# Performance work log

Hardware: AMD Instinct MI355X
Metric: run time of the kernel (lower is better)

The kernel has to match this reference:

```python
import jax, jax.numpy as jnp
import numpy as np

LOG2PI = float(np.log(2.0 * np.pi))
T, S, D, K = 1024, 512, 32, 64


def setup_inputs() -> dict:
    key = jax.random.key(0)
    k0, k1, k2, k3, k4 = jax.random.split(key, 5)
    data = jax.random.normal(k0, (T, S, D), dtype=jnp.float32)  # packed time-major
    ip = jax.random.uniform(k1, (K,), dtype=jnp.float32)
    initial_probs = ip / ip.sum()
    A = jax.random.uniform(k2, (K, K), dtype=jnp.float32)
    transition_probs = A / A.sum(-1, keepdims=True)  # row-stochastic
    means = jax.random.normal(k3, (K, D), dtype=jnp.float32)
    covars = jax.random.uniform(k4, (K, D), dtype=jnp.float32) * 0.5 + 0.5  # positive diag
    return {"data": data, "initial_probs": initial_probs,
            "transition_probs": transition_probs, "means": means, "covars": covars}


def _emission_probs(data, means, covars):
    # Gaussian diag-covariance densities, [T, S, K], without materializing [T,S,K,D].
    inv = 1.0 / covars  # [K, D]
    quad = (jnp.einsum('tsd,kd->tsk', data * data, inv)
            - 2.0 * jnp.einsum('tsd,kd->tsk', data, means * inv)
            + (means * means * inv).sum(-1))  # [T, S, K]
    logp = -0.5 * (quad + jnp.log(covars).sum(-1) + data.shape[-1] * LOG2PI)
    return jnp.exp(logp)


def reference(data, initial_probs, transition_probs, means, covars):
    probs = _emission_probs(data, means, covars)  # [T, S, K]
    # t = 0: alpha = normalize(initial * emission)
    a0 = initial_probs * probs[0]
    d0 = a0.sum(-1, keepdims=True)
    alpha0 = a0 / d0
    log_denom0 = jnp.log(d0)  # [S, 1]

    def step(carry, p_t):
        alpha, log_denom = carry
        a = p_t * (alpha @ transition_probs)  # [S, K]
        d = a.sum(-1, keepdims=True)
        return (a / d, log_denom + jnp.log(d)), None

    (alpha, log_denom), _ = jax.lax.scan(step, (alpha0, log_denom0), probs[1:])
    log_likeli = jax.nn.logsumexp(jnp.log(alpha) + log_denom, axis=-1).sum()
    return alpha, -log_likeli
```

## Files before the change

kernel.cpp:

```cpp
#include <hip/hip_runtime.h>
#include <hip/hip_fp16.h>
#include <math.h>

#define TT 1024
#define SS 512
#define DD 32
#define KK 64

#define LOG2PI_F 1.8378770664093453f

#define NSEG 4
#define SEGLEN (TT / NSEG)
#define BURN 64


typedef float v2f __attribute__((ext_vector_type(2)));

__device__ __forceinline__ v2f fma2(v2f a, v2f b, v2f c) {
#if __has_builtin(__builtin_elementwise_fma)
    return __builtin_elementwise_fma(a, b, c);
#else
    v2f r; r.x = fmaf(a.x, b.x, c.x); r.y = fmaf(a.y, b.y, c.y); return r;
#endif
}

__device__ __forceinline__ void pin2(v2f& v) { asm volatile("" : "+v"(v)); }

template <int CTRL, int RMASK>
__device__ __forceinline__ float dpp_add(float x) {
    int t = __builtin_amdgcn_update_dpp(0, __float_as_int(x), CTRL, RMASK, 0xf, true);
    return x + __int_as_float(t);
}
template <int CTRL, int RMASK>
__device__ __forceinline__ float dpp_max(float x) {
    int xi = __float_as_int(x);
    int t = __builtin_amdgcn_update_dpp(xi, xi, CTRL, RMASK, 0xf, false);
    return fmaxf(x, __int_as_float(t));
}
__device__ __forceinline__ float wave_reduce_sum(float x) {
    x = dpp_add<0x111, 0xf>(x);
    x = dpp_add<0x112, 0xf>(x);
    x = dpp_add<0x114, 0xf>(x);
    x = dpp_add<0x118, 0xf>(x);
    x = dpp_add<0x142, 0xa>(x);
    x = dpp_add<0x143, 0xc>(x);
    return __int_as_float(__builtin_amdgcn_readlane(__float_as_int(x), 63));
}
__device__ __forceinline__ float wave_reduce_max(float x) {
    x = dpp_max<0x111, 0xf>(x);
    x = dpp_max<0x112, 0xf>(x);
    x = dpp_max<0x114, 0xf>(x);
    x = dpp_max<0x118, 0xf>(x);
    x = dpp_max<0x142, 0xa>(x);
    x = dpp_max<0x143, 0xc>(x);
    return __int_as_float(__builtin_amdgcn_readlane(__float_as_int(x), 63));
}

__global__ __launch_bounds__(64)
__attribute__((amdgpu_waves_per_eu(1, 2)))
void hmm_fused(
    const float* __restrict__ data,
    const float* __restrict__ initial,
    const float* __restrict__ trans,
    const float* __restrict__ means,
    const float* __restrict__ covars,
    float* __restrict__ out_alpha,
    float* __restrict__ seq_logd)
{
    const int s   = blockIdx.x;
    const int seg = blockIdx.y;
    const int k   = threadIdx.x;

    const int emit_from = seg * SEGLEN;
    const int t0        = seg ? (emit_from - BURN) : 0;
    const int nsteps    = seg ? (SEGLEN + BURN) : SEGLEN;

    v2f w2[DD / 2], m2[DD / 2];
    float c0 = DD * LOG2PI_F;
#pragma unroll
    for (int d = 0; d < DD; ++d) {
        float c = covars[k * DD + d];
        ((float*)w2)[d] = 1.0f / c;
        ((float*)m2)[d] = means[k * DD + d];
        c0 += __logf(c);
    }
#pragma unroll
    for (int j = 0; j < DD / 2; ++j) { pin2(w2[j]); pin2(m2[j]); }

    v2f acl[KK / 2];
#pragma unroll
    for (int j = 0; j < KK / 2; ++j) {
        acl[j].x = trans[(2 * j) * KK + k];
        acl[j].y = trans[(2 * j + 1) * KK + k];
    }
#pragma unroll
    for (int j = 0; j < KK / 2; ++j) pin2(acl[j]);

    __shared__ __align__(16) float alpha_sh[KK];

    float4 xA[DD / 4], xB[DD / 4];
    {
        const float4* xp = (const float4*)(data + ((size_t)t0 * SS + s) * DD);
#pragma unroll
        for (int j = 0; j < DD / 4; ++j) xA[j] = xp[j];
    }

    const float init_k = seg ? 1.0f : initial[k];
    float logd = 0.0f;
    float macc = 0.0f;
    float a = 0.0f;
    float scl = 1.0f;

#define FUSED_STEP(XCUR, XNXT, Ii)                                            \
    {                                                                         \
        const int t = t0 + 8 * mblk + (Ii);                                   \
        int tn = t + 1; if (tn >= TT) tn = TT - 1;         \
        const float4* xp =                                                    \
            (const float4*)(data + ((size_t)tn * SS + s) * DD);               \
        _Pragma("unroll")                                                     \
        for (int j = 0; j < DD / 4; ++j) XNXT[j] = xp[j];                     \
               \
        v2f q0 = {0.0f, 0.0f}, q1 = {0.0f, 0.0f};                             \
        _Pragma("unroll")                                                     \
        for (int d4 = 0; d4 < DD / 4; ++d4) {                                 \
            float4 x = XCUR[d4];                                              \
            v2f xa; xa.x = x.x; xa.y = x.y;                                   \
            v2f xb; xb.x = x.z; xb.y = x.w;                                   \
            v2f ta = xa - m2[2 * d4];                                         \
            v2f tb = xb - m2[2 * d4 + 1];                                     \
            q0 = fma2(w2[2 * d4] * ta, ta, q0);                               \
            q1 = fma2(w2[2 * d4 + 1] * tb, tb, q1);                           \
        }                                                                     \
        float qq = (q0.x + q0.y) + (q1.x + q1.y);                             \
        float logp = -0.5f * (qq + c0);                                       \
        float mx = wave_reduce_max(logp);              \
        float pc = __expf(logp - mx);                                         \
        if (((Ii) & 3) == 0) pc *= scl;            \
        if (t >= emit_from) macc += mx;                                       \
            \
        if ((Ii) == 0 && mblk == 0) {                                         \
            a = init_k * pc;                                                  \
        } else {                                                              \
            const float4* ash4 = (const float4*)alpha_sh;                     \
            v2f a0 = {0,0}, a1 = {0,0}, a2 = {0,0}, a3 = {0,0};               \
            _Pragma("unroll")                                                 \
            for (int j4 = 0; j4 < KK / 4; ++j4) {                             \
                float4 av = ash4[j4];                                         \
                v2f lo; lo.x = av.x; lo.y = av.y;                             \
                v2f hi; hi.x = av.z; hi.y = av.w;                             \
                if (j4 & 1) {                                                 \
                    a2 = fma2(lo, acl[2 * j4], a2);                           \
                    a3 = fma2(hi, acl[2 * j4 + 1], a3);                       \
                } else {                                                      \
                    a0 = fma2(lo, acl[2 * j4], a0);                           \
                    a1 = fma2(hi, acl[2 * j4 + 1], a1);                       \
                }                                                             \
            }                                                                 \
            v2f sv = (a0 + a1) + (a2 + a3);                                   \
            a = pc * (sv.x + sv.y);                                           \
        }                                                                     \
        alpha_sh[k] = a;                    \
        __builtin_amdgcn_wave_barrier();   \
        if (((Ii) & 3) == 3) {                \
            float den = wave_reduce_sum(a);                                   \
            logd += (t >= emit_from) ? __logf(den) : 0.0f;                    \
            scl = __builtin_amdgcn_rcpf(den);                                 \
        }                                                                     \
    }

    for (int mblk = 0; mblk < nsteps / 8; ++mblk) {
        FUSED_STEP(xA, xB, 0)
        FUSED_STEP(xB, xA, 1)
        FUSED_STEP(xA, xB, 2)
        FUSED_STEP(xB, xA, 3)
        FUSED_STEP(xA, xB, 4)
        FUSED_STEP(xB, xA, 5)
        FUSED_STEP(xA, xB, 6)
        FUSED_STEP(xB, xA, 7)
    }
#undef FUSED_STEP

    if (seg == NSEG - 1) out_alpha[(size_t)s * KK + k] = a * scl;
    if (k == 0) seq_logd[seg * SS + s] = logd + macc;
}

__global__ __launch_bounds__(256) void finalize(
    const float* __restrict__ seq_logd, float* __restrict__ out_nll)
{
    float v = 0.0f;
    for (int j = threadIdx.x; j < NSEG * SS; j += 256) v += seq_logd[j];
#pragma unroll
    for (int off = 32; off > 0; off >>= 1)
        v += __shfl_xor(v, off, 64);
    __shared__ float sh[4];
    if ((threadIdx.x & 63) == 0) sh[threadIdx.x >> 6] = v;
    __syncthreads();
    if (threadIdx.x == 0) {
        double total = ((double)sh[0] + sh[1]) + ((double)sh[2] + sh[3]);
        out_nll[0] = (float)(-total);
    }
}

extern "C" void kernel_launch(void* const* d_in, const int* in_sizes, int n_in,
                              void* d_out, int out_size, void* d_ws, size_t ws_size,
                              hipStream_t stream) {
    const float* data    = (const float*)d_in[0];
    const float* initial = (const float*)d_in[1];
    const float* trans   = (const float*)d_in[2];
    const float* means   = (const float*)d_in[3];
    const float* covars  = (const float*)d_in[4];

    float* out_alpha = (float*)d_out;
    float* out_nll   = (float*)d_out + (size_t)SS * KK;

    float* seq_logd = (float*)d_ws;

    hmm_fused<<<dim3(SS, NSEG), 64, 0, stream>>>(
        data, initial, trans, means, covars, out_alpha, seq_logd);
    finalize<<<1, 256, 0, stream>>>(seq_logd, out_nll);
}
```

Baseline: 301.3 us.

## Use readlane broadcast for alpha matvec and stage data through LDS double buffer

The alpha-times-transition matvec now broadcasts alpha with v_readlane from registers instead of writing it to shared memory and reading it back as float4. Each block of 8 timesteps of observation data is loaded cooperatively by the whole wave into a double-buffered LDS tile, replacing per-lane redundant float4 global loads. The segment count drops from 4 to 2 and the kernel is restricted to one wave per EU. This removes the LDS round trip and the redundant global traffic, but readlane produces scalar values, so the matvec may serialize through SGPRs. Fewer segments also means less parallelism and longer sequential chains per block.

Result: slower. 488.6 us (+62.2%).

```diff
diff --git a/kernel.cpp b/kernel.cpp
--- a/kernel.cpp
+++ b/kernel.cpp
@@ -1,5 +1,4 @@
 #include <hip/hip_runtime.h>
-#include <hip/hip_fp16.h>
 #include <math.h>
 
 #define TT 1024
@@ -9,7 +8,7 @@
 
 #define LOG2PI_F 1.8378770664093453f
 
-#define NSEG 4
+#define NSEG 2
 #define SEGLEN (TT / NSEG)
 #define BURN 64
 
@@ -25,6 +24,7 @@
 }
 
 __device__ __forceinline__ void pin2(v2f& v) { asm volatile("" : "+v"(v)); }
+__device__ __forceinline__ void pinf(float& v) { asm volatile("" : "+v"(v)); }
 
 template <int CTRL, int RMASK>
 __device__ __forceinline__ float dpp_add(float x) {
@@ -57,7 +57,7 @@
 }
 
 __global__ __launch_bounds__(64)
-__attribute__((amdgpu_waves_per_eu(1, 2)))
+__attribute__((amdgpu_waves_per_eu(1, 1)))
 void hmm_fused(
     const float* __restrict__ data,
     const float* __restrict__ initial,
@@ -87,43 +87,53 @@
 #pragma unroll
     for (int j = 0; j < DD / 2; ++j) { pin2(w2[j]); pin2(m2[j]); }
 
-    v2f acl[KK / 2];
-#pragma unroll
-    for (int j = 0; j < KK / 2; ++j) {
-        acl[j].x = trans[(2 * j) * KK + k];
-        acl[j].y = trans[(2 * j + 1) * KK + k];
-    }
-#pragma unroll
-    for (int j = 0; j < KK / 2; ++j) pin2(acl[j]);
-
-    __shared__ __align__(16) float alpha_sh[KK];
-
-    float4 xA[DD / 4], xB[DD / 4];
-    {
-        const float4* xp = (const float4*)(data + ((size_t)t0 * SS + s) * DD);
-#pragma unroll
-        for (int j = 0; j < DD / 4; ++j) xA[j] = xp[j];
-    }
+    float aclf[KK];
+#pragma unroll
+    for (int j = 0; j < KK; ++j) aclf[j] = trans[j * KK + k];
+#pragma unroll
+    for (int j = 0; j < KK; ++j) pinf(aclf[j]);
+
+    __shared__ __align__(16) float xlds[2][8 * DD];
+
+    const int half = k >> 5, d_lane = k & 31;
+    const float* xptr = data + (size_t)s * DD + (size_t)half * SS * DD + d_lane;
+
+    float xr0, xr1, xr2, xr3;
+#define XLOAD(TB)                                                             \
+    {                                                                         \
+        size_t bb = (size_t)(TB) * (SS * DD);                                 \
+        xr0 = xptr[bb];                                                       \
+        xr1 = xptr[bb + 2 * (SS * DD)];                                       \
+        xr2 = xptr[bb + 4 * (SS * DD)];                                       \
+        xr3 = xptr[bb + 6 * (SS * DD)];                                       \
+    }
+#define XWRITE(BUF)                                                           \
+    {                                                                         \
+        xlds[BUF][k]       = xr0;                                             \
+        xlds[BUF][64 + k]  = xr1;                                             \
+        xlds[BUF][128 + k] = xr2;                                             \
+        xlds[BUF][192 + k] = xr3;                                             \
+    }
+
+    XLOAD(t0);
+    XWRITE(0);
 
     const float init_k = seg ? 1.0f : initial[k];
     float logd = 0.0f;
     float macc = 0.0f;
     float a = 0.0f;
     float scl = 1.0f;
-
-#define FUSED_STEP(XCUR, XNXT, Ii)                                            \
+    int cur = 0;
+
+#define FUSED_STEP(Ii)                                                        \
     {                                                                         \
-        const int t = t0 + 8 * mblk + (Ii);                                   \
-        int tn = t + 1; if (tn >= TT) tn = TT - 1;         \
-        const float4* xp =                                                    \
-            (const float4*)(data + ((size_t)tn * SS + s) * DD);               \
-        _Pragma("unroll")                                                     \
-        for (int j = 0; j < DD / 4; ++j) XNXT[j] = xp[j];                     \
+        const int t = tbase + (Ii);                                           \
+        const float4* xq = (const float4*)(xcur + (Ii) * DD);                 \
                \
         v2f q0 = {0.0f, 0.0f}, q1 = {0.0f, 0.0f};                             \
         _Pragma("unroll")                                                     \
         for (int d4 = 0; d4 < DD / 4; ++d4) {                                 \
-            float4 x = XCUR[d4];                                              \
+            float4 x = xq[d4];                                                \
             v2f xa; xa.x = x.x; xa.y = x.y;                                   \
             v2f xb; xb.x = x.z; xb.y = x.w;                                   \
             v2f ta = xa - m2[2 * d4];                                         \
@@ -137,30 +147,25 @@
         float pc = __expf(logp - mx);                                         \
         if (((Ii) & 3) == 0) pc *= scl;            \
         if (t >= emit_from) macc += mx;                                       \
-            \
+                    \
         if ((Ii) == 0 && mblk == 0) {                                         \
             a = init_k * pc;                                                  \
         } else {                                                              \
-            const float4* ash4 = (const float4*)alpha_sh;                     \
-            v2f a0 = {0,0}, a1 = {0,0}, a2 = {0,0}, a3 = {0,0};               \
+            const int ai = __float_as_int(a);                                 \
+            float ac0 = 0.0f, ac1 = 0.0f, ac2 = 0.0f, ac3 = 0.0f;             \
             _Pragma("unroll")                                                 \
-            for (int j4 = 0; j4 < KK / 4; ++j4) {                             \
-                float4 av = ash4[j4];                                         \
-                v2f lo; lo.x = av.x; lo.y = av.y;                             \
-                v2f hi; hi.x = av.z; hi.y = av.w;                             \
-                if (j4 & 1) {                                                 \
-                    a2 = fma2(lo, acl[2 * j4], a2);                           \
-                    a3 = fma2(hi, acl[2 * j4 + 1], a3);                       \
-                } else {                                                      \
-                    a0 = fma2(lo, acl[2 * j4], a0);                           \
-                    a1 = fma2(hi, acl[2 * j4 + 1], a1);                       \
-                }                                                             \
+            for (int j = 0; j < KK; j += 4) {                                 \
+                ac0 = fmaf(__int_as_float(__builtin_amdgcn_readlane(ai, j + 0)), \
+                           aclf[j + 0], ac0);                                 \
+                ac1 = fmaf(__int_as_float(__builtin_amdgcn_readlane(ai, j + 1)), \
+                           aclf[j + 1], ac1);                                 \
+                ac2 = fmaf(__int_as_float(__builtin_amdgcn_readlane(ai, j + 2)), \
+                           aclf[j + 2], ac2);                                 \
+                ac3 = fmaf(__int_as_float(__builtin_amdgcn_readlane(ai, j + 3)), \
+                           aclf[j + 3], ac3);                                 \
             }                                                                 \
-            v2f sv = (a0 + a1) + (a2 + a3);                                   \
-            a = pc * (sv.x + sv.y);                                           \
+            a = pc * ((ac0 + ac1) + (ac2 + ac3));                             \
         }                                                                     \
-        alpha_sh[k] = a;                    \
-        __builtin_amdgcn_wave_barrier();   \
         if (((Ii) & 3) == 3) {                \
             float den = wave_reduce_sum(a);                                   \
             logd += (t >= emit_from) ? __logf(den) : 0.0f;                    \
@@ -169,16 +174,25 @@
     }
 
     for (int mblk = 0; mblk < nsteps / 8; ++mblk) {
-        FUSED_STEP(xA, xB, 0)
-        FUSED_STEP(xB, xA, 1)
-        FUSED_STEP(xA, xB, 2)
-        FUSED_STEP(xB, xA, 3)
-        FUSED_STEP(xA, xB, 4)
-        FUSED_STEP(xB, xA, 5)
-        FUSED_STEP(xA, xB, 6)
-        FUSED_STEP(xB, xA, 7)
+        const int tbase = t0 + 8 * mblk;
+        int tb_next = tbase + 8;
+        if (tb_next > TT - 8) tb_next = TT - 8;
+        XLOAD(tb_next);
+        const float* xcur = xlds[cur];
+        FUSED_STEP(0)
+        FUSED_STEP(1)
+        FUSED_STEP(2)
+        FUSED_STEP(3)
+        FUSED_STEP(4)
+        FUSED_STEP(5)
+        FUSED_STEP(6)
+        FUSED_STEP(7)
+        XWRITE(cur ^ 1);
+        cur ^= 1;
     }
 #undef FUSED_STEP
+#undef XLOAD
+#undef XWRITE
 
     if (seg == NSEG - 1) out_alpha[(size_t)s * KK + k] = a * scl;
     if (k == 0) seq_logd[seg * SS + s] = logd + macc;
```
